# Kernel optimization log

Hardware: AMD Instinct MI355X
Metric: run time of the kernel (lower is better)

## Reference

```python
import jax, jax.numpy as jnp
import numpy as np

TEMPERATURE = 16.0  # sqrt(d_k) for d_k=256

def setup_inputs() -> dict:
    key = jax.random.key(0)
    q = jax.random.normal(key, (32, 1024, 256), dtype=jnp.float32)
    return {"q": q}

def reference(q):
    # attn = q @ q^T  (b, l, l)
    attn = jnp.einsum('bld,bmd->blm', q, q)
    # data-dependent zero mask -> -inf fill (before temperature scaling, matching torch order)
    zero_mask = attn == 0.0
    attn = jnp.where(zero_mask, -jnp.inf, attn / TEMPERATURE)
    attn = jax.nn.softmax(attn, axis=2)
    # rows that were fully -inf produce NaN -> zero them out
    attn = jnp.where(jnp.isnan(attn), 0.0, attn)
    # dropout is identity in eval/reference mode
    output = jnp.einsum('blm,bmd->bld', attn, q)
    return (output, attn)
```

## Files before the change

kernel.cpp:

```cpp
#include <hip/hip_runtime.h>
#include <stdint.h>

#define NB 32
#define NL 1024
#define ND 256

typedef __attribute__((ext_vector_type(8))) __bf16 bf16x8;
typedef __attribute__((ext_vector_type(4))) float f32x4;

__device__ __forceinline__ uint16_t f2bf(float f) {
  union { float f; uint32_t u; } v; v.f = f;
  return (uint16_t)((v.u + 0x7fffu + ((v.u >> 16) & 1u)) >> 16);
}

#define GLD_LDS16(g, l)                                                        \
  __builtin_amdgcn_global_load_lds(                                            \
      (__attribute__((address_space(1))) void*)(g),                            \
      (__attribute__((address_space(3))) void*)(l), 16, 0, 0)

__global__ __launch_bounds__(256) void convert_kernel(
    const float* __restrict__ q, uint16_t* __restrict__ qb,
    uint16_t* __restrict__ qt) {
  __shared__ uint16_t tile[64][72];
  int b = blockIdx.z;
  int l0 = blockIdx.x * 64, d0 = blockIdx.y * 64;
  int t = threadIdx.x;
  int r = t >> 4;
  int c4 = (t & 15) * 4;
  const float* qsrc = q + (size_t)b * NL * ND;
  uint16_t* qbb = qb + (size_t)b * NL * ND;
  uint16_t* qtb = qt + (size_t)b * ND * NL;
#pragma unroll
  for (int i = 0; i < 4; i++) {
    int row = r + 16 * i;
    float4 v = *(const float4*)(qsrc + (size_t)(l0 + row) * ND + d0 + c4);
    ushort4 h;
    h.x = f2bf(v.x); h.y = f2bf(v.y); h.z = f2bf(v.z); h.w = f2bf(v.w);
    *(ushort4*)(qbb + (size_t)(l0 + row) * ND + d0 + c4) = h;
    tile[row][c4 + 0] = h.x; tile[row][c4 + 1] = h.y;
    tile[row][c4 + 2] = h.z; tile[row][c4 + 3] = h.w;
  }
  __syncthreads();
#pragma unroll
  for (int i = 0; i < 4; i++) {
    int drow = r + 16 * i;
    ushort4 h;
    h.x = tile[c4 + 0][drow]; h.y = tile[c4 + 1][drow];
    h.z = tile[c4 + 2][drow]; h.w = tile[c4 + 3][drow];
    *(ushort4*)(qtb + (size_t)(d0 + drow) * NL + l0 + c4) = h;
  }
}

__global__ __launch_bounds__(256) void qk_kernel(
    const uint16_t* __restrict__ qb, float* __restrict__ e_out) {
  __shared__ alignas(16) uint16_t As[128 * 32];
  __shared__ alignas(16) uint16_t Bs[128 * 32];
  int b = blockIdx.z;
  int m0 = blockIdx.x * 128, n0 = blockIdx.y * 128;
  const uint16_t* Q = qb + (size_t)b * NL * ND;
  int tid = threadIdx.x, lane = tid & 63, wave = tid >> 6;
  int wm = (wave & 1) * 64, wn = (wave >> 1) * 64;
  int quad = lane >> 4, l15 = lane & 15;
  f32x4 acc[4][4] = {};

  for (int k0 = 0; k0 < ND; k0 += 32) {
    __syncthreads();
#pragma unroll
    for (int i = 0; i < 2; i++) {
      int c = i * 256 + wave * 64 + lane;
      int row = c >> 2, cc = c & 3;
      int sw = (row >> 1) & 3;
      int gc = k0 + ((cc ^ sw) * 8);
      GLD_LDS16(Q + (size_t)(m0 + row) * ND + gc,
                As + (size_t)(i * 256 + wave * 64) * 8);
      GLD_LDS16(Q + (size_t)(n0 + row) * ND + gc,
                Bs + (size_t)(i * 256 + wave * 64) * 8);
    }
    __syncthreads();
    bf16x8 af[4], bfr[4];
#pragma unroll
    for (int t = 0; t < 4; t++) {
      int ra = wm + t * 16 + l15;
      af[t] = *(const bf16x8*)(As + ra * 32 + ((quad ^ ((ra >> 1) & 3)) * 8));
      int rb = wn + t * 16 + l15;
      bfr[t] = *(const bf16x8*)(Bs + rb * 32 + ((quad ^ ((rb >> 1) & 3)) * 8));
    }
#pragma unroll
    for (int tm = 0; tm < 4; tm++)
#pragma unroll
      for (int tn = 0; tn < 4; tn++)
        acc[tm][tn] = __builtin_amdgcn_mfma_f32_16x16x32_bf16(
            af[tm], bfr[tn], acc[tm][tn], 0, 0, 0);
  }

  const float k = 0.09016844005555f;
  float* Eb = e_out + (size_t)b * NL * NL;
#pragma unroll
  for (int tm = 0; tm < 4; tm++) {
    int rbase = m0 + wm + tm * 16 + quad * 4;
#pragma unroll
    for (int tn = 0; tn < 4; tn++) {
      int col = n0 + wn + tn * 16 + l15;
#pragma unroll
      for (int j = 0; j < 4; j++) {
        float s = acc[tm][tn][j];
        float e = (s == 0.0f) ? 0.0f : __builtin_amdgcn_exp2f(s * k);
        Eb[(size_t)(rbase + j) * NL + col] = e;
      }
    }
  }
}

__global__ __launch_bounds__(256) void norm_kernel(float* __restrict__ attn) {
  __shared__ float red[4];
  float* p = attn + (size_t)blockIdx.x * NL;
  int t = threadIdx.x;
  float4 v = *(float4*)(p + t * 4);
  float s = v.x + v.y + v.z + v.w;
#pragma unroll
  for (int off = 32; off > 0; off >>= 1) s += __shfl_down(s, off, 64);
  int wave = t >> 6, lane = t & 63;
  if (lane == 0) red[wave] = s;
  __syncthreads();
  float total = red[0] + red[1] + red[2] + red[3];
  float inv = (total > 0.0f) ? 1.0f / total : 0.0f;
  v.x *= inv; v.y *= inv; v.z *= inv; v.w *= inv;
  *(float4*)(p + t * 4) = v;
}

__global__ __launch_bounds__(256) void pv_kernel(
    const float* __restrict__ attn, const uint16_t* __restrict__ qt,
    float* __restrict__ out) {
  __shared__ alignas(16) uint16_t As[128 * 40];
  __shared__ alignas(16) uint16_t Bs[128 * 32];
  int b = blockIdx.z;
  int m0 = blockIdx.x * 128, d0 = blockIdx.y * 128;
  const float* A = attn + (size_t)b * NL * NL;
  const uint16_t* Bt = qt + (size_t)b * ND * NL;
  int tid = threadIdx.x, lane = tid & 63, wave = tid >> 6;
  int wm = (wave & 1) * 64, wn = (wave >> 1) * 64;
  int quad = lane >> 4, l15 = lane & 15;
  f32x4 acc[4][4] = {};

  for (int k0 = 0; k0 < NL; k0 += 32) {
    __syncthreads();
#pragma unroll
    for (int i = 0; i < 2; i++) {
      int c = i * 256 + wave * 64 + lane;
      int row = c >> 2, cc = c & 3;
      int sw = (row >> 1) & 3;
      GLD_LDS16(Bt + (size_t)(d0 + row) * NL + k0 + ((cc ^ sw) * 8),
                Bs + (size_t)(i * 256 + wave * 64) * 8);
    }
#pragma unroll
    for (int j = 0; j < 4; j++) {
      int f = tid + j * 256;
      int row = f >> 3, c4 = (f & 7) * 4;
      float4 v = *(const float4*)(A + (size_t)(m0 + row) * NL + k0 + c4);
      ushort4 h;
      h.x = f2bf(v.x); h.y = f2bf(v.y); h.z = f2bf(v.z); h.w = f2bf(v.w);
      *(ushort4*)(&As[row * 40 + c4]) = h;
    }
    __syncthreads();
    bf16x8 af[4], bfr[4];
#pragma unroll
    for (int t = 0; t < 4; t++) {
      int ra = wm + t * 16 + l15;
      af[t] = *(const bf16x8*)(&As[ra * 40 + quad * 8]);
      int rb = wn + t * 16 + l15;
      bfr[t] = *(const bf16x8*)(&Bs[rb * 32 + ((quad ^ ((rb >> 1) & 3)) * 8)]);
    }
#pragma unroll
    for (int tm = 0; tm < 4; tm++)
#pragma unroll
      for (int tn = 0; tn < 4; tn++)
        acc[tm][tn] = __builtin_amdgcn_mfma_f32_16x16x32_bf16(
            af[tm], bfr[tn], acc[tm][tn], 0, 0, 0);
  }

  float* O = out + (size_t)b * NL * ND;
#pragma unroll
  for (int tm = 0; tm < 4; tm++) {
    int rbase = m0 + wm + tm * 16 + quad * 4;
#pragma unroll
    for (int tn = 0; tn < 4; tn++) {
      int col = d0 + wn + tn * 16 + l15;
#pragma unroll
      for (int j = 0; j < 4; j++)
        O[(size_t)(rbase + j) * ND + col] = acc[tm][tn][j];
    }
  }
}

extern "C" void kernel_launch(void* const* d_in, const int* in_sizes, int n_in,
                              void* d_out, int out_size, void* d_ws,
                              size_t ws_size, hipStream_t stream) {
  (void)in_sizes; (void)n_in; (void)out_size; (void)ws_size;
  const float* q = (const float*)d_in[0];
  float* out = (float*)d_out;
  float* attn = out + (size_t)NB * NL * ND;
  uint16_t* qb = (uint16_t*)d_ws;
  uint16_t* qt = qb + (size_t)NB * NL * ND;

  convert_kernel<<<dim3(16, 4, NB), 256, 0, stream>>>(q, qb, qt);
  qk_kernel<<<dim3(8, 8, NB), 256, 0, stream>>>(qb, attn);
  norm_kernel<<<NB * NL, 256, 0, stream>>>(attn);
  pv_kernel<<<dim3(8, 2, NB), 256, 0, stream>>>(attn, qt, out);
}
```

Baseline: 289.7 us.

## Store unnormalized bf16 exp in attn buffer, fuse row sums and defer normalization

The QK kernel now writes bf16 exponentials into the first half of each fp32 attention row and puts per-tile partial row sums in the upper half. The PV kernel loads the bf16 tile directly through global-to-LDS copies and applies the row reciprocal in its epilogue. A final scale kernel widens to fp32 and normalizes in place. This removes the separate fp32 normalization pass and the fp32 read and convert in PV, but stores attn through bf16 and relies on in-place aliasing within each row, where the bf16 data sits entirely before the partial sums.

```diff
diff --git a/kernel.cpp b/kernel.cpp
--- a/kernel.cpp
+++ b/kernel.cpp
@@ -4,6 +4,7 @@
 #define NB 32
 #define NL 1024
 #define ND 256
+#define ROWU16 2048
 
 typedef __attribute__((ext_vector_type(8))) __bf16 bf16x8;
 typedef __attribute__((ext_vector_type(4))) float f32x4;
@@ -11,6 +12,10 @@
 __device__ __forceinline__ uint16_t f2bf(float f) {
   union { float f; uint32_t u; } v; v.f = f;
   return (uint16_t)((v.u + 0x7fffu + ((v.u >> 16) & 1u)) >> 16);
+}
+__device__ __forceinline__ float bf2f(uint16_t h) {
+  union { uint32_t u; float f; } v; v.u = ((uint32_t)h) << 16;
+  return v.f;
 }
 
 #define GLD_LDS16(g, l)                                                        \
@@ -52,9 +57,10 @@
 }
 
 __global__ __launch_bounds__(256) void qk_kernel(
-    const uint16_t* __restrict__ qb, float* __restrict__ e_out) {
+    const uint16_t* __restrict__ qb, float* __restrict__ attn_f32) {
   __shared__ alignas(16) uint16_t As[128 * 32];
   __shared__ alignas(16) uint16_t Bs[128 * 32];
+  __shared__ float rp[128][2];
   int b = blockIdx.z;
   int m0 = blockIdx.x * 128, n0 = blockIdx.y * 128;
   const uint16_t* Q = qb + (size_t)b * NL * ND;
@@ -93,55 +99,63 @@
             af[tm], bfr[tn], acc[tm][tn], 0, 0, 0);
   }
 
-  const float k = 0.09016844005555f;
-  float* Eb = e_out + (size_t)b * NL * NL;
+  const float kf = 0.09016844005555f;
+  uint16_t* attn_u16 = (uint16_t*)attn_f32;
+  size_t gbase = (size_t)b * NL;
 #pragma unroll
   for (int tm = 0; tm < 4; tm++) {
-    int rbase = m0 + wm + tm * 16 + quad * 4;
+    int rbl = wm + tm * 16 + quad * 4;
+    float rsum[4] = {0.f, 0.f, 0.f, 0.f};
 #pragma unroll
     for (int tn = 0; tn < 4; tn++) {
       int col = n0 + wn + tn * 16 + l15;
 #pragma unroll
       for (int j = 0; j < 4; j++) {
         float s = acc[tm][tn][j];
-        float e = (s == 0.0f) ? 0.0f : __builtin_amdgcn_exp2f(s * k);
-        Eb[(size_t)(rbase + j) * NL + col] = e;
+        float e = (s == 0.0f) ? 0.0f : __builtin_amdgcn_exp2f(s * kf);
+        attn_u16[(gbase + m0 + rbl + j) * ROWU16 + col] = f2bf(e);
+        rsum[j] += e;
       }
     }
-  }
-}
-
-__global__ __launch_bounds__(256) void norm_kernel(float* __restrict__ attn) {
-  __shared__ float red[4];
-  float* p = attn + (size_t)blockIdx.x * NL;
-  int t = threadIdx.x;
-  float4 v = *(float4*)(p + t * 4);
-  float s = v.x + v.y + v.z + v.w;
-#pragma unroll
-  for (int off = 32; off > 0; off >>= 1) s += __shfl_down(s, off, 64);
-  int wave = t >> 6, lane = t & 63;
-  if (lane == 0) red[wave] = s;
+#pragma unroll
+    for (int j = 0; j < 4; j++) {
+      float v = rsum[j];
+      v += __shfl_xor(v, 1, 64);
+      v += __shfl_xor(v, 2, 64);
+      v += __shfl_xor(v, 4, 64);
+      v += __shfl_xor(v, 8, 64);
+      if (l15 == 0) rp[rbl + j][wave >> 1] = v;
+    }
+  }
   __syncthreads();
-  float total = red[0] + red[1] + red[2] + red[3];
-  float inv = (total > 0.0f) ? 1.0f / total : 0.0f;
-  v.x *= inv; v.y *= inv; v.z *= inv; v.w *= inv;
-  *(float4*)(p + t * 4) = v;
+  if (tid < 128) {
+    float s = rp[tid][0] + rp[tid][1];
+    attn_f32[(gbase + m0 + tid) * (size_t)NL + 512 + blockIdx.y] = s;
+  }
 }
 
 __global__ __launch_bounds__(256) void pv_kernel(
-    const float* __restrict__ attn, const uint16_t* __restrict__ qt,
+    const float* __restrict__ attn_f32, const uint16_t* __restrict__ qt,
     float* __restrict__ out) {
-  __shared__ alignas(16) uint16_t As[128 * 40];
+  __shared__ alignas(16) uint16_t As[128 * 32];
   __shared__ alignas(16) uint16_t Bs[128 * 32];
+  __shared__ float inv_lds[128];
   int b = blockIdx.z;
   int m0 = blockIdx.x * 128, d0 = blockIdx.y * 128;
-  const float* A = attn + (size_t)b * NL * NL;
+  const uint16_t* Ap = (const uint16_t*)attn_f32 + (size_t)b * NL * ROWU16;
   const uint16_t* Bt = qt + (size_t)b * ND * NL;
   int tid = threadIdx.x, lane = tid & 63, wave = tid >> 6;
   int wm = (wave & 1) * 64, wn = (wave >> 1) * 64;
   int quad = lane >> 4, l15 = lane & 15;
   f32x4 acc[4][4] = {};
 
+  if (tid < 128) {
+    const float* pf =
+        attn_f32 + (size_t)(b * NL + m0 + tid) * NL + 512;
+    float s = pf[0] + pf[1] + pf[2] + pf[3] + pf[4] + pf[5] + pf[6] + pf[7];
+    inv_lds[tid] = (s > 0.0f) ? 1.0f / s : 0.0f;
+  }
+
   for (int k0 = 0; k0 < NL; k0 += 32) {
     __syncthreads();
 #pragma unroll
@@ -149,26 +163,20 @@
       int c = i * 256 + wave * 64 + lane;
       int row = c >> 2, cc = c & 3;
       int sw = (row >> 1) & 3;
-      GLD_LDS16(Bt + (size_t)(d0 + row) * NL + k0 + ((cc ^ sw) * 8),
+      int gc = k0 + ((cc ^ sw) * 8);
+      GLD_LDS16(Ap + (size_t)(m0 + row) * ROWU16 + gc,
+                As + (size_t)(i * 256 + wave * 64) * 8);
+      GLD_LDS16(Bt + (size_t)(d0 + row) * NL + gc,
                 Bs + (size_t)(i * 256 + wave * 64) * 8);
-    }
-#pragma unroll
-    for (int j = 0; j < 4; j++) {
-      int f = tid + j * 256;
-      int row = f >> 3, c4 = (f & 7) * 4;
-      float4 v = *(const float4*)(A + (size_t)(m0 + row) * NL + k0 + c4);
-      ushort4 h;
-      h.x = f2bf(v.x); h.y = f2bf(v.y); h.z = f2bf(v.z); h.w = f2bf(v.w);
-      *(ushort4*)(&As[row * 40 + c4]) = h;
     }
     __syncthreads();
     bf16x8 af[4], bfr[4];
 #pragma unroll
     for (int t = 0; t < 4; t++) {
       int ra = wm + t * 16 + l15;
-      af[t] = *(const bf16x8*)(&As[ra * 40 + quad * 8]);
+      af[t] = *(const bf16x8*)(As + ra * 32 + ((quad ^ ((ra >> 1) & 3)) * 8));
       int rb = wn + t * 16 + l15;
-      bfr[t] = *(const bf16x8*)(&Bs[rb * 32 + ((quad ^ ((rb >> 1) & 3)) * 8)]);
+      bfr[t] = *(const bf16x8*)(Bs + rb * 32 + ((quad ^ ((rb >> 1) & 3)) * 8));
     }
 #pragma unroll
     for (int tm = 0; tm < 4; tm++)
@@ -181,15 +189,31 @@
   float* O = out + (size_t)b * NL * ND;
 #pragma unroll
   for (int tm = 0; tm < 4; tm++) {
-    int rbase = m0 + wm + tm * 16 + quad * 4;
+    int rbl = wm + tm * 16 + quad * 4;
 #pragma unroll
     for (int tn = 0; tn < 4; tn++) {
       int col = d0 + wn + tn * 16 + l15;
 #pragma unroll
       for (int j = 0; j < 4; j++)
-        O[(size_t)(rbase + j) * ND + col] = acc[tm][tn][j];
-    }
-  }
+        O[(size_t)(m0 + rbl + j) * ND + col] = acc[tm][tn][j] * inv_lds[rbl + j];
+    }
+  }
+}
+
+__global__ __launch_bounds__(256) void scale_kernel(float* __restrict__ attn_f32) {
+  size_t g = blockIdx.x;
+  const uint16_t* u = (const uint16_t*)attn_f32 + g * ROWU16;
+  float* f = attn_f32 + g * (size_t)NL;
+  int t = threadIdx.x;
+  ushort4 h = ((const ushort4*)u)[t];
+  float s = f[512] + f[513] + f[514] + f[515] +
+            f[516] + f[517] + f[518] + f[519];
+  float inv = (s > 0.0f) ? 1.0f / s : 0.0f;
+  __syncthreads();
+  float4 v;
+  v.x = bf2f(h.x) * inv; v.y = bf2f(h.y) * inv;
+  v.z = bf2f(h.z) * inv; v.w = bf2f(h.w) * inv;
+  ((float4*)f)[t] = v;
 }
 
 extern "C" void kernel_launch(void* const* d_in, const int* in_sizes, int n_in,
@@ -204,6 +228,6 @@
 
   convert_kernel<<<dim3(16, 4, NB), 256, 0, stream>>>(q, qb, qt);
   qk_kernel<<<dim3(8, 8, NB), 256, 0, stream>>>(qb, attn);
-  norm_kernel<<<NB * NL, 256, 0, stream>>>(attn);
   pv_kernel<<<dim3(8, 2, NB), 256, 0, stream>>>(attn, qt, out);
-}
+  scale_kernel<<<NB * NL, 256, 0, stream>>>(attn);
+}
```

Result: faster. 271.1 us (-6.4%).
